# Performance work log

Measured on AMD Instinct MI355X. Metric: run time of the kernel, lower is better.

Reference implementation:

```python
import jax, jax.numpy as jnp
import numpy as np

NEURAL_DIM = 512
N_UNITS = 512
N_DAYS = 24
N_CLASSES = 41
N_LAYERS = 5
PATCH = 14
STRIDE = 4
MEMORY_SIZE = 256
IN0 = NEURAL_DIM * PATCH  # 7168, layer-0 input after patch concat


def _expm(M):
    """Matrix exponential via scaling-and-squaring + Taylor (float64 numpy)."""
    nrm = np.linalg.norm(M, 1)
    s = max(0, int(np.ceil(np.log2(nrm))) + 4) if nrm > 0 else 0
    Ms = M / (2.0 ** s)
    n = M.shape[0]
    E = np.eye(n)
    term = np.eye(n)
    for k in range(1, 25):
        term = term @ Ms / k
        E = E + term
    for _ in range(s):
        E = E @ E
    return E


def _lmu_AB(m_size):
    # NOTE: the torch cell calls _compute_A_B(memory_size, B.shape[0]), so the
    # effective theta used for discretization is memory_size itself.
    theta = float(m_size)
    q = np.arange(m_size, dtype=np.float64)
    R = ((2.0 * q + 1.0) / theta).reshape(-1, 1)
    i, j = np.meshgrid(q, q, indexing='ij')
    A = R * np.where(i < j, -1.0, (-1.0) ** (i - j + 1))
    Bc = R * ((-1.0) ** q).reshape(-1, 1)
    # zero-order hold discretization with dt=1: expm([[A,B],[0,0]])
    aug = np.zeros((m_size + 1, m_size + 1))
    aug[:m_size, :m_size] = A
    aug[:m_size, m_size:] = Bc
    E = _expm(aug)
    return (jnp.asarray(E[:m_size, :m_size], dtype=jnp.float32),
            jnp.asarray(E[:m_size, m_size:], dtype=jnp.float32))


A_MAT, B_MAT = _lmu_AB(MEMORY_SIZE)  # [M,M], [M,1]


def setup_inputs() -> dict:
    key = jax.random.key(0)
    ks = jax.random.split(key, 20)

    def rn(k, shape, scale):
        return jax.random.normal(k, shape, dtype=jnp.float32) * scale

    inp = {
        'x': jax.random.normal(ks[0], (32, 1024, NEURAL_DIM), dtype=jnp.float32),
        'day_idx': jax.random.randint(ks[1], (32,), 0, N_DAYS),
        # day-specific input layers (init: identity + zero bias; perturb slightly)
        'day_W': jnp.broadcast_to(jnp.eye(NEURAL_DIM, dtype=jnp.float32), (N_DAYS, NEURAL_DIM, NEURAL_DIM)) + rn(ks[2], (N_DAYS, NEURAL_DIM, NEURAL_DIM), 0.01),
        'day_b': rn(ks[3], (N_DAYS, 1, NEURAL_DIM), 0.01),
        # layer 0 (input 7168)
        'e_x0': rn(ks[4], (1, IN0), 1.0 / np.sqrt(IN0)),
        'W_x0': rn(ks[5], (N_UNITS, IN0), np.sqrt(2.0 / (IN0 + N_UNITS))),
        # layers 1..4 (input 512)
        'e_xr': rn(ks[6], (N_LAYERS - 1, 1, N_UNITS), 1.0 / np.sqrt(N_UNITS)),
        'W_xr': rn(ks[7], (N_LAYERS - 1, N_UNITS, N_UNITS), np.sqrt(1.0 / N_UNITS)),
        # shared-shape per-layer params (stacked over 5 layers)
        'e_h': rn(ks[8], (N_LAYERS, 1, N_UNITS), 1.0 / np.sqrt(N_UNITS)),
        'e_m': rn(ks[9], (N_LAYERS, 1, MEMORY_SIZE), 0.02),
        'W_h': rn(ks[10], (N_LAYERS, N_UNITS, N_UNITS), np.sqrt(1.0 / N_UNITS)),
        'W_m': rn(ks[11], (N_LAYERS, N_UNITS, MEMORY_SIZE), np.sqrt(2.0 / (MEMORY_SIZE + N_UNITS))),
        'h0': rn(ks[12], (N_LAYERS, 1, N_UNITS), 0.05),
        'm0': rn(ks[13], (N_LAYERS, 1, MEMORY_SIZE), 0.05),
        'out_W': rn(ks[14], (N_CLASSES, N_UNITS), np.sqrt(2.0 / (N_UNITS + N_CLASSES))),
        'out_b': jnp.zeros((N_CLASSES,), dtype=jnp.float32),
    }
    return inp


def _run_lmu_layer(seq, e_x, W_x, e_h, e_m, W_h, W_m, h_init, m_init):
    """seq: [B,T,in] -> [B,T,H] LMU recurrence."""
    # precompute input projections (the only big GEMMs) outside the scan
    xWx = jnp.einsum('bti,hi->bth', seq, W_x)   # [B,T,H]
    xex = jnp.einsum('bti,oi->bto', seq, e_x)   # [B,T,1]

    def step(carry, inp):
        h, m = carry
        xw, xe = inp
        u = xe + h @ e_h.T + m @ e_m.T          # [B,1]
        m = m @ A_MAT.T + u @ B_MAT.T           # [B,M]
        h = jnp.tanh(xw + h @ W_h.T + m @ W_m.T)
        return (h, m), h

    (_, _), hs = jax.lax.scan(step, (h_init, m_init),
                              (jnp.swapaxes(xWx, 0, 1), jnp.swapaxes(xex, 0, 1)))
    return jnp.swapaxes(hs, 0, 1)  # [B,T,H]


def reference(x, day_idx, day_W, day_b, e_x0, W_x0, e_xr, W_xr,
              e_h, e_m, W_h, W_m, h0, m0, out_W, out_b):
    B = x.shape[0]
    # day-specific linear + softsign
    h = jnp.einsum('btd,bdk->btk', x, day_W[day_idx]) + day_b[day_idx]
    h = h / (1.0 + jnp.abs(h))  # Softsign
    # patch concat: unfold time dim with window=PATCH, stride=STRIDE
    T = h.shape[1]
    Tp = (T - PATCH) // STRIDE + 1
    idx = jnp.arange(Tp)[:, None] * STRIDE + jnp.arange(PATCH)[None, :]
    h = h[:, idx, :].reshape(B, Tp, PATCH * NEURAL_DIM)  # [B,Tp,7168]

    bc = lambda v, d: jnp.broadcast_to(v, (B, d))
    seq = _run_lmu_layer(h, e_x0, W_x0, e_h[0], e_m[0], W_h[0], W_m[0],
                         bc(h0[0], N_UNITS), bc(m0[0], MEMORY_SIZE))
    for i in range(1, N_LAYERS):
        seq = _run_lmu_layer(seq, e_xr[i - 1], W_xr[i - 1], e_h[i], e_m[i],
                             W_h[i], W_m[i], bc(h0[i], N_UNITS), bc(m0[i], MEMORY_SIZE))
    logits = seq @ out_W.T + out_b  # [B,Tp,n_classes]
    return logits
```

## Files before the change

kernel.cpp:

```cpp
#include <hip/hip_runtime.h>
#include <hip/hip_fp16.h>

typedef _Float16 f16;
typedef _Float16 f16x8 __attribute__((ext_vector_type(8)));
typedef float f32x4 __attribute__((ext_vector_type(4)));

#define DI static __device__ __forceinline__

constexpr int N2 = 257 * 257;
#define LSTRIDE ((size_t)254 * 32 * 768)

DI f32x4 mfma16(f16x8 a, f16x8 b, f32x4 c) {
  return __builtin_amdgcn_mfma_f32_16x16x32_f16(a, b, c, 0, 0, 0);
}
DI f16x8 ldg8(const f16* p) { return *reinterpret_cast<const f16x8*>(p); }
DI f16x8 cvt8(const float* s) {
  f16x8 v;
#pragma unroll
  for (int j = 0; j < 8; ++j) v[j] = (f16)s[j];
  return v;
}
DI double invfact(int k) {
  double f = 1.0;
  for (int i = 2; i <= k; ++i) f *= (double)i;
  return 1.0 / f;
}

DI void st_d_sc1(double* p, double v) {
  asm volatile("global_store_dwordx2 %0, %1, off sc1" :: "v"(p), "v"(v) : "memory");
}
DI void st_f_sc1(float* p, float v) {
  asm volatile("global_store_dword %0, %1, off sc1" :: "v"(p), "v"(v) : "memory");
}
DI void st_h_sc1(f16* p, f16 v) {
  asm volatile("global_store_short %0, %1, off sc1" :: "v"(p), "v"(v) : "memory");
}
DI int ld_llc(const int* p) {
  return __hip_atomic_load(p, __ATOMIC_RELAXED, __HIP_MEMORY_SCOPE_AGENT);
}
DI void add_llc(int* p) {
  __hip_atomic_fetch_add(p, 1, __ATOMIC_RELAXED, __HIP_MEMORY_SCOPE_AGENT);
}
DI void drain_vm() { asm volatile("s_waitcnt vmcnt(0)" ::: "memory"); }
DI void membar() {
  __builtin_amdgcn_sched_barrier(0);
  asm volatile("" ::: "memory");
}
DI void spin_ge(const int* p, int target) {
  for (int it = 0; it < (1 << 14); ++it) {
    if (ld_llc(p) >= target) return;
    __builtin_amdgcn_s_sleep(1);
  }
}
DI void st4_sc1(f16* b, f16 v0, f16 v1, f16 v2, f16 v3) {
  const f16* b2 = b + 1536;
  asm volatile(
      "global_store_short %4, %0, off sc1\n\t"
      "global_store_short %4, %1, off offset:1536 sc1\n\t"
      "global_store_short %5, %2, off sc1\n\t"
      "global_store_short %5, %3, off offset:1536 sc1\n\t"
      "s_waitcnt vmcnt(0)"
      :: "v"(v0), "v"(v1), "v"(v2), "v"(v3), "v"(b), "v"(b2) : "memory");
}

DI void gridbar_nf(int* bar, int nwg) {
  drain_vm();
  __syncthreads();
  if (threadIdx.x == 0) {
    int g = ld_llc(bar + 1);
    int old = __hip_atomic_fetch_add(bar, 1, __ATOMIC_RELAXED, __HIP_MEMORY_SCOPE_AGENT);
    if (old == nwg - 1) {
      __hip_atomic_store(bar, 0, __ATOMIC_RELAXED, __HIP_MEMORY_SCOPE_AGENT);
      add_llc(bar + 1);
    } else {
      for (int it = 0; it < (1 << 14) && ld_llc(bar + 1) == g; ++it)
        __builtin_amdgcn_s_sleep(1);
    }
  }
  __syncthreads();
}

DI void mm257(double* __restrict__ D, const double* __restrict__ A, const double* __restrict__ Bm,
              int fj, const double* __restrict__ T1, const double* __restrict__ T2,
              const double* __restrict__ T3, int gtid, int nth) {
  double c0 = 0, c1 = 0, c2 = 0, c3 = 0;
  if (fj >= 0) {
    c0 = invfact(4 * fj); c1 = invfact(4 * fj + 1);
    c2 = invfact(4 * fj + 2); c3 = invfact(4 * fj + 3);
  }
  for (int e = gtid; e < N2; e += nth) {
    int i = e / 257, j = e - i * 257;
    const double* ar = A + (size_t)i * 257;
    const double* bc = Bm + j;
    double s0 = 0, s1 = 0, s2 = 0, s3 = 0;
    for (int k = 0; k < 256; k += 4) {
      s0 = fma(ar[k], bc[(size_t)k * 257], s0);
      s1 = fma(ar[k + 1], bc[(size_t)(k + 1) * 257], s1);
      s2 = fma(ar[k + 2], bc[(size_t)(k + 2) * 257], s2);
      s3 = fma(ar[k + 3], bc[(size_t)(k + 3) * 257], s3);
    }
    double s = ((s0 + s1) + (s2 + s3)) + ar[256] * bc[(size_t)256 * 257];
    if (fj >= 0) s += c0 * ((i == j) ? 1.0 : 0.0) + c1 * T1[e] + c2 * T2[e] + c3 * T3[e];
    st_d_sc1(D + e, s);
  }
}

__global__ __launch_bounds__(256) void k_setup(
    const float* __restrict__ dayW, const float* __restrict__ ex0, const float* __restrict__ Wx0,
    const float* __restrict__ exr, const float* __restrict__ Wxr,
    const float* __restrict__ eh, const float* __restrict__ em,
    const float* __restrict__ Wh, const float* __restrict__ Wm, const float* __restrict__ outW,
    double* __restrict__ X, float* __restrict__ w1f, float* __restrict__ AWt,
    float* __restrict__ btf, f16* __restrict__ gbuf, f16* __restrict__ wxcat,
    f16* __restrict__ outw, f16* __restrict__ dayWt, int* __restrict__ bar) {
  const int gtid = blockIdx.x * 256 + threadIdx.x;
  const int nth = 128 * 256;
  double* Ms = X;
  double* M2 = X + N2;
  double* M3 = X + 2 * N2;
  double* M4 = X + 3 * N2;
  double* H = X + 4 * N2;
  double* S = X + 11 * N2;

  for (int e = gtid; e < N2; e += nth) {
    int i = e / 257, j = e - i * 257;
    double v = 0.0;
    if (i < 256) {
      double R = (2.0 * i + 1.0) / 256.0;
      if (j < 256) v = R * ((i < j) ? -1.0 : (((i - j) & 1) ? 1.0 : -1.0));
      else v = R * ((i & 1) ? -1.0 : 1.0);
    }
    st_d_sc1(Ms + e, v / 64.0);
  }
  for (int e = gtid; e < 576 * 896; e += nth) {
    int n = e / 896, kc = (e - n * 896) * 8;
    f16x8 v;
    if (n < 512) v = cvt8(Wx0 + (size_t)n * 7168 + kc);
    else if (n == 512) v = cvt8(ex0 + kc);
    else {
#pragma unroll
      for (int j = 0; j < 8; ++j) v[j] = (f16)0.f;
    }
    *reinterpret_cast<f16x8*>(wxcat + (size_t)n * 7168 + kc) = v;
  }
  for (int e = gtid; e < 48 * 64; e += nth) {
    int n = e / 64, kc = (e - n * 64) * 8;
    f16x8 v;
    if (n < 41) v = cvt8(outW + (size_t)n * 512 + kc);
    else {
#pragma unroll
      for (int j = 0; j < 8; ++j) v[j] = (f16)0.f;
    }
    *reinterpret_cast<f16x8*>(outw + (size_t)n * 512 + kc) = v;
  }
  {
    __shared__ float tile[64][65];
    for (int tt = blockIdx.x; tt < 24 * 64; tt += 128) {
      int D = tt >> 6; int r = tt & 63; int kb = (r >> 3) * 64; int nb = (r & 7) * 64;
      __syncthreads();
      for (int q = 0; q < 16; ++q) {
        int idx = threadIdx.x + q * 256; int kk = idx >> 6; int nn = idx & 63;
        tile[kk][nn] = dayW[(size_t)D * 262144 + (size_t)(kb + kk) * 512 + nb + nn];
      }
      __syncthreads();
      for (int q = 0; q < 2; ++q) {
        int cidx = threadIdx.x + q * 256; int nn = cidx >> 3; int kc = (cidx & 7) * 8;
        f16x8 v;
#pragma unroll
        for (int jj = 0; jj < 8; ++jj) v[jj] = (f16)tile[kc + jj][nn];
        *reinterpret_cast<f16x8*>(dayWt + (size_t)D * 262144 + (size_t)(nb + nn) * 512 + kb + kc) = v;
      }
    }
    __syncthreads();
  }
  gridbar_nf(bar, 128);

  mm257(M2, Ms, Ms, -1, Ms, Ms, Ms, gtid, nth); gridbar_nf(bar, 128);
  mm257(M3, M2, Ms, -1, Ms, Ms, Ms, gtid, nth); gridbar_nf(bar, 128);
  mm257(M4, M2, M2, -1, Ms, Ms, Ms, gtid, nth);
  for (int e = gtid; e < N2; e += nth) {
    int i = e / 257, j = e - i * 257;
    st_d_sc1(H + e, (i == j) ? invfact(24) : 0.0);
  }
  gridbar_nf(bar, 128);
  for (int k = 0; k < 6; ++k) {
    mm257(H + (size_t)(k + 1) * N2, H + (size_t)k * N2, M4, 5 - k, Ms, M2, M3, gtid, nth);
    gridbar_nf(bar, 128);
  }
  {
    const double* Ssrc = H + (size_t)6 * N2;
    for (int k = 0; k < 6; ++k) {
      mm257(S + (size_t)k * N2, Ssrc, Ssrc, -1, Ms, Ms, Ms, gtid, nth);
      gridbar_nf(bar, 128);
      Ssrc = S + (size_t)k * N2;
    }
  }
  const double* E = S + (size_t)5 * N2;

  for (int e = gtid; e < 256; e += nth) st_f_sc1(btf + e, (float)E[(size_t)e * 257 + 256]);
  for (int e = gtid; e < 5 * 512; e += nth) {
    int l = e / 512, n = e - l * 512;
    const float* wm = Wm + ((size_t)l * 512 + n) * 256;
    float s = 0.f;
    for (int j = 0; j < 256; ++j) s += (float)E[(size_t)j * 257 + 256] * wm[j];
    st_f_sc1(w1f + e, s);
  }
  for (int e = gtid; e < 5 * 512 * 256; e += nth) {
    int l = e / (512 * 256); int r = e - l * 512 * 256; int n = r >> 8; int i = r & 255;
    const double* Ec = E + i;
    const float* wm = Wm + ((size_t)l * 512 + n) * 256;
    float s0 = 0, s1 = 0, s2 = 0, s3 = 0;
    for (int j = 0; j < 256; j += 4) {
      s0 += (float)Ec[(size_t)j * 257] * wm[j];
      s1 += (float)Ec[(size_t)(j + 1) * 257] * wm[j + 1];
      s2 += (float)Ec[(size_t)(j + 2) * 257] * wm[j + 2];
      s3 += (float)Ec[(size_t)(j + 3) * 257] * wm[j + 3];
    }
    st_f_sc1(AWt + e, (s0 + s1) + (s2 + s3));
  }
  gridbar_nf(bar, 128);

  for (int e = gtid; e < 5 * 768 * 160; e += nth) {
    int l = e / (768 * 160); int r = e - l * 768 * 160; int n = r / 160; int k = (r - n * 160) * 8;
    if (l == 0 && k >= 768) continue;
    f16x8 v;
    if (n < 512) {
      float w1n = w1f[l * 512 + n];
      if (k < 512) {
        const float* a = Wh + ((size_t)l * 512 + n) * 512 + k;
        const float* b = eh + (size_t)l * 512 + k;
#pragma unroll
        for (int jj = 0; jj < 8; ++jj) v[jj] = (f16)(a[jj] + b[jj] * w1n);
      } else if (k < 768) {
        int i = k - 512;
        const float* a = AWt + ((size_t)l * 512 + n) * 256 + i;
        const float* b = em + (size_t)l * 256 + i;
#pragma unroll
        for (int jj = 0; jj < 8; ++jj) v[jj] = (f16)(a[jj] + b[jj] * w1n);
      } else {
        int d = k - 768;
        const float* a = Wxr + ((size_t)(l - 1) * 512 + n) * 512 + d;
        const float* b = exr + (size_t)(l - 1) * 512 + d;
#pragma unroll
        for (int jj = 0; jj < 8; ++jj) v[jj] = (f16)(a[jj] + b[jj] * w1n);
      }
    } else {
      int jm = n - 512;
      float btn = btf[jm];
      if (k < 512) {
        const float* b = eh + (size_t)l * 512 + k;
#pragma unroll
        for (int jj = 0; jj < 8; ++jj) v[jj] = (f16)(b[jj] * btn);
      } else if (k < 768) {
        int i = k - 512;
        const double* a = E + (size_t)jm * 257 + i;
        const float* b = em + (size_t)l * 256 + i;
#pragma unroll
        for (int jj = 0; jj < 8; ++jj) v[jj] = (f16)((float)a[jj] + b[jj] * btn);
      } else {
        int d = k - 768;
        const float* b = exr + (size_t)(l - 1) * 512 + d;
#pragma unroll
        for (int jj = 0; jj < 8; ++jj) v[jj] = (f16)(b[jj] * btn);
      }
    }
    *reinterpret_cast<f16x8*>(gbuf + ((size_t)l * 768 + n) * 1280 + k) = v;
  }
}

__global__ __launch_bounds__(256) void k_day(const float* __restrict__ x,
    const int* __restrict__ dayIdx, const float* __restrict__ dayb,
    const f16* __restrict__ dayWt, f16* __restrict__ h1) {
  __shared__ f16 As[64][40];
  __shared__ f16 Bs[256][40];
  const int bid = blockIdx.x;
  const int b = bid >> 5; const int r = bid & 31;
  const int t0 = (r >> 1) * 64; const int n0 = (r & 1) * 256;
  const int D = dayIdx[b];
  const int tid = threadIdx.x, lane = tid & 63, w = tid >> 6, q4 = lane >> 4;
  const float* xb = x + ((size_t)b * 1024 + t0) * 512;
  const f16* Wt = dayWt + (size_t)D * 262144 + (size_t)n0 * 512;
  f32x4 acc[16];
#pragma unroll
  for (int i = 0; i < 16; ++i) acc[i] = (f32x4){0.f, 0.f, 0.f, 0.f};
  for (int kt = 0; kt < 16; ++kt) {
    const int k0 = kt * 32;
    __syncthreads();
    { int row = tid >> 2, c8 = (tid & 3) * 8;
      *reinterpret_cast<f16x8*>(&As[row][c8]) = cvt8(xb + (size_t)row * 512 + k0 + c8); }
    for (int q = 0; q < 4; ++q) {
      int idx = tid + q * 256; int row = idx >> 2; int c8 = (idx & 3) * 8;
      *reinterpret_cast<f16x8*>(&Bs[row][c8]) = ldg8(Wt + (size_t)row * 512 + k0 + c8);
    }
    __syncthreads();
    f16x8 a = *reinterpret_cast<const f16x8*>(&As[w * 16 + (lane & 15)][q4 * 8]);
#pragma unroll
    for (int nt2 = 0; nt2 < 16; ++nt2) {
      f16x8 bb = *reinterpret_cast<const f16x8*>(&Bs[nt2 * 16 + (lane & 15)][q4 * 8]);
      acc[nt2] = mfma16(a, bb, acc[nt2]);
    }
  }
#pragma unroll
  for (int nt2 = 0; nt2 < 16; ++nt2) {
    int n = n0 + nt2 * 16 + (lane & 15);
    float db = dayb[(size_t)D * 512 + n];
#pragma unroll
    for (int i = 0; i < 4; ++i) {
      int t = t0 + w * 16 + q4 * 4 + i;
      float v = acc[nt2][i] + db;
      v = v / (1.f + fabsf(v));
      h1[((size_t)b * 1024 + t) * 512 + n] = (f16)v;
    }
  }
}

__global__ __launch_bounds__(256) void k_xw0(const f16* __restrict__ h1,
    const f16* __restrict__ wxcat, float* __restrict__ xw0) {
  __shared__ f16 As[128][40];
  __shared__ f16 Bs[96][40];
  const int bid = blockIdx.x;
  const int mt = bid / 6; const int nb = bid - mt * 6;
  const int m0 = mt * 128; const int n0 = nb * 96;
  const int tid = threadIdx.x, lane = tid & 63, w = tid >> 6, q4 = lane >> 4;
  f32x4 acc[2][6];
#pragma unroll
  for (int a = 0; a < 2; ++a)
#pragma unroll
    for (int b = 0; b < 6; ++b) acc[a][b] = (f32x4){0.f, 0.f, 0.f, 0.f};
  for (int kt = 0; kt < 224; ++kt) {
    const int k0 = kt * 32; const int p = k0 >> 9; const int kd = k0 & 511;
    __syncthreads();
    for (int q = 0; q < 2; ++q) {
      int idx = tid + q * 256; int row = idx >> 2; int c8 = (idx & 3) * 8;
      int m = m0 + row; int b = m >> 8; int tp = m & 255; if (tp > 252) tp = 252;
      *reinterpret_cast<f16x8*>(&As[row][c8]) =
          ldg8(h1 + ((size_t)b * 1024 + (size_t)tp * 4 + p) * 512 + kd + c8);
    }
    for (int q = 0; q < 2; ++q) {
      int idx = tid + q * 256;
      if (idx < 384) {
        int row = idx >> 2; int c8 = (idx & 3) * 8;
        *reinterpret_cast<f16x8*>(&Bs[row][c8]) =
            ldg8(wxcat + (size_t)(n0 + row) * 7168 + k0 + c8);
      }
    }
    __syncthreads();
#pragma unroll
    for (int mb = 0; mb < 2; ++mb) {
      f16x8 a = *reinterpret_cast<const f16x8*>(&As[w * 32 + mb * 16 + (lane & 15)][q4 * 8]);
#pragma unroll
      for (int nt2 = 0; nt2 < 6; ++nt2) {
        f16x8 bb = *reinterpret_cast<const f16x8*>(&Bs[nt2 * 16 + (lane & 15)][q4 * 8]);
        acc[mb][nt2] = mfma16(a, bb, acc[mb][nt2]);
      }
    }
  }
#pragma unroll
  for (int mb = 0; mb < 2; ++mb)
#pragma unroll
    for (int nt2 = 0; nt2 < 6; ++nt2)
#pragma unroll
      for (int i = 0; i < 4; ++i) {
        int m = m0 + w * 32 + mb * 16 + q4 * 4 + i;
        int n = n0 + nt2 * 16 + (lane & 15);
        xw0[(size_t)m * 576 + n] = acc[mb][nt2][i];
      }
}

template <int KK>
DI void rec_run(int l, int c, int tid, const f16* __restrict__ gbuf, f16* __restrict__ sbuf,
                const float* __restrict__ xw0, const float* __restrict__ w1f,
                const float* __restrict__ btf, const float* __restrict__ h0,
                const float* __restrict__ m0, int* done, f16* bflds) {
  const int lane = tid & 63, w = tid >> 6;
  const int mb = w / 3, nt = w % 3;
  const int nbase = c * 48 + nt * 16;
  const int ncol = nbase + (lane & 15);
  const int q4 = lane >> 4;

  for (int r = tid; r < 32 * 48; r += 384) {
    int row = r / 48; int col = c * 48 + (r - row * 48);
    float v = (col < 512) ? h0[(size_t)l * 512 + col] : m0[(size_t)l * 256 + col - 512];
    st_h_sc1(sbuf + (size_t)l * LSTRIDE + (size_t)row * 768 + col, (f16)v);
  }

  const f16* gb = gbuf + ((size_t)l * 768 + ncol) * 1280 + (size_t)q4 * 8;
  constexpr int NREG = (KK > 32) ? 32 : KK;
  f16x8 bf[NREG];
#pragma unroll
  for (int kk = 0; kk < NREG; ++kk) bf[kk] = ldg8(gb + (size_t)kk * 32);
  if (KK == 40) {
#pragma unroll
    for (int kk = 32; kk < 40; ++kk) {
      f16x8 v = ldg8(gb + (size_t)kk * 32);
      *reinterpret_cast<f16x8*>(bflds + ((size_t)(w * 8 + (kk - 32)) * 64 + lane) * 8) = v;
    }
  }
  float w1n = 0.f, btn = 0.f;
  if (KK == 24) {
    if (ncol < 512) w1n = w1f[ncol];
    else btn = btf[ncol - 512];
  }
  drain_vm();
  __syncthreads();
  if (tid == 0) add_llc(done + l * 256);

  for (int t = 0; t < 253; ++t) {
    if (tid == 0) {
      spin_ge(done + l * 256 + t, 16);
      if (l > 0) spin_ge(done + (l - 1) * 256 + t + 1, 16);
    }
    __builtin_amdgcn_s_barrier();
    membar();

    const int arow = mb * 16 + (lane & 15);
    const f16* s0 = sbuf + (size_t)l * LSTRIDE + ((size_t)t * 32 + arow) * 768 + (size_t)q4 * 8;
    f32x4 acc = {0.f, 0.f, 0.f, 0.f};
#pragma unroll
    for (int kk = 0; kk < 24; ++kk) acc = mfma16(ldg8(s0 + (size_t)kk * 32), bf[kk < NREG ? kk : 0], acc);
    if (KK == 40) {
      const f16* s1 = sbuf + (size_t)(l - 1) * LSTRIDE + ((size_t)(t + 1) * 32 + arow) * 768 + (size_t)q4 * 8;
#pragma unroll
      for (int kk = 24; kk < 32; ++kk) acc = mfma16(ldg8(s1 + (size_t)(kk - 24) * 32), bf[kk < NREG ? kk : 0], acc);
#pragma unroll
      for (int kk = 32; kk < 40; ++kk) {
        f16x8 bb = *reinterpret_cast<const f16x8*>(bflds + ((size_t)(w * 8 + (kk - 32)) * 64 + lane) * 8);
        acc = mfma16(ldg8(s1 + (size_t)(kk - 24) * 32), bb, acc);
      }
    }

    f16 v4[4];
#pragma unroll
    for (int i = 0; i < 4; ++i) {
      const int brow = mb * 16 + q4 * 4 + i;
      float v = acc[i];
      if (KK == 24) {
        const float* xr = xw0 + ((size_t)brow * 256 + t) * 576;
        float xe = xr[512];
        v += (ncol < 512) ? (xr[ncol] + xe * w1n) : (xe * btn);
      }
      if (ncol < 512) v = tanhf(v);
      v4[i] = (f16)v;
    }
    f16* dst = sbuf + (size_t)l * LSTRIDE +
               ((size_t)(t + 1) * 32 + (size_t)(mb * 16 + q4 * 4)) * 768 + ncol;
    st4_sc1(dst, v4[0], v4[1], v4[2], v4[3]);

    __builtin_amdgcn_s_barrier();
    if (tid == 0) add_llc(done + l * 256 + t + 1);
  }
}

__global__ __launch_bounds__(384, 2) void k_rec(const f16* __restrict__ gbuf, f16* __restrict__ sbuf,
    const float* __restrict__ xw0, const float* __restrict__ w1f,
    const float* __restrict__ btf, const float* __restrict__ h0,
    const float* __restrict__ m0, int* __restrict__ done) {
  __shared__ f16 bflds[6 * 8 * 64 * 8];
  const int l = blockIdx.x >> 4;
  const int c = blockIdx.x & 15;
  if (l == 0)
    rec_run<24>(0, c, threadIdx.x, gbuf, sbuf, xw0, w1f, btf, h0, m0, done, bflds);
  else
    rec_run<40>(l, c, threadIdx.x, gbuf, sbuf, xw0, w1f, btf, h0, m0, done, bflds);
}

__global__ __launch_bounds__(256) void k_out(const f16* __restrict__ sbuf4,
    const f16* __restrict__ outw, const float* __restrict__ outb, float* __restrict__ out) {
  const int bid = blockIdx.x; const int b = bid >> 2; const int tp0 = (bid & 3) * 64;
  const int tid = threadIdx.x, lane = tid & 63, w = tid >> 6, q4 = lane >> 4;
  f32x4 acc[3];
#pragma unroll
  for (int i = 0; i < 3; ++i) acc[i] = (f32x4){0.f, 0.f, 0.f, 0.f};
  int tq = tp0 + w * 16 + (lane & 15) + 1;
  const int tau = tq > 253 ? 253 : tq;
  const f16* arow = sbuf4 + ((size_t)tau * 32 + b) * 768 + (size_t)q4 * 8;
#pragma unroll
  for (int kk = 0; kk < 16; ++kk) {
    f16x8 a = ldg8(arow + (size_t)kk * 32);
#pragma unroll
    for (int nt2 = 0; nt2 < 3; ++nt2) {
      f16x8 bb = ldg8(outw + (size_t)(nt2 * 16 + (lane & 15)) * 512 + kk * 32 + q4 * 8);
      acc[nt2] = mfma16(a, bb, acc[nt2]);
    }
  }
#pragma unroll
  for (int nt2 = 0; nt2 < 3; ++nt2) {
    int cc = nt2 * 16 + (lane & 15);
    if (cc < 41) {
      float ob = outb[cc];
#pragma unroll
      for (int i = 0; i < 4; ++i) {
        int tp = tp0 + w * 16 + q4 * 4 + i;
        if (tp < 253) out[((size_t)b * 253 + tp) * 41 + cc] = acc[nt2][i] + ob;
      }
    }
  }
}

extern "C" void kernel_launch(void* const* d_in, const int* in_sizes, int n_in,
                              void* d_out, int out_size, void* d_ws, size_t ws_size,
                              hipStream_t stream) {
  const float* x      = (const float*)d_in[0];
  const int*   dayIdx = (const int*)d_in[1];
  const float* day_W  = (const float*)d_in[2];
  const float* day_b  = (const float*)d_in[3];
  const float* e_x0   = (const float*)d_in[4];
  const float* W_x0   = (const float*)d_in[5];
  const float* e_xr   = (const float*)d_in[6];
  const float* W_xr   = (const float*)d_in[7];
  const float* e_h    = (const float*)d_in[8];
  const float* e_m    = (const float*)d_in[9];
  const float* W_h    = (const float*)d_in[10];
  const float* W_m    = (const float*)d_in[11];
  const float* h0     = (const float*)d_in[12];
  const float* m0     = (const float*)d_in[13];
  const float* out_W  = (const float*)d_in[14];
  const float* out_b  = (const float*)d_in[15];
  float* outp = (float*)d_out;

  char* w = (char*)d_ws;
  size_t o = 0;
  auto al = [&](size_t n) { void* p = w + o; o = (o + n + 255) & ~(size_t)255; return p; };

  int*   flags = (int*)  al(16384);
  f16*   gbuf  = (f16*)  al((size_t)5 * 768 * 1280 * 2);
  f16*   outw  = (f16*)  al((size_t)48 * 512 * 2);
  float* xw0   = (float*)al((size_t)8192 * 576 * 4);
  float* w1f   = (float*)al((size_t)5 * 512 * 4);
  float* btf   = (float*)al(256 * 4);

  const size_t XB    = ((size_t)17 * N2 * 8 + 255) & ~(size_t)255;
  const size_t AWTB  = ((size_t)5 * 512 * 256 * 4 + 255) & ~(size_t)255;
  const size_t DAYB  = ((size_t)24 * 512 * 512 * 2 + 255) & ~(size_t)255;
  const size_t WXB   = ((size_t)576 * 7168 * 2 + 255) & ~(size_t)255;
  const size_t H1B   = ((size_t)32 * 1024 * 512 * 2 + 255) & ~(size_t)255;
  const size_t SBUFB = (size_t)5 * LSTRIDE * 2;
  size_t ovb = XB + AWTB + DAYB + WXB + H1B;
  if (SBUFB > ovb) ovb = SBUFB;
  char* ov = (char*)al(ovb);
  double* X     = (double*)ov;
  float*  AWt   = (float*)(ov + XB);
  f16*    dayWt = (f16*)(ov + XB + AWTB);
  f16*    wxcat = (f16*)(ov + XB + AWTB + DAYB);
  f16*    h1    = (f16*)(ov + XB + AWTB + DAYB + WXB);
  f16*    sbuf  = (f16*)ov;

  if (o > ws_size) return;
  (void)in_sizes; (void)n_in; (void)out_size;

  hipMemsetAsync(flags, 0, 16384, stream);
  k_setup<<<128, 256, 0, stream>>>(day_W, e_x0, W_x0, e_xr, W_xr, e_h, e_m, W_h, W_m,
                                   out_W, X, w1f, AWt, btf, gbuf, wxcat, outw, dayWt,
                                   flags + 2048);
  k_day<<<1024, 256, 0, stream>>>(x, dayIdx, day_b, dayWt, h1);
  k_xw0<<<384, 256, 0, stream>>>(h1, wxcat, xw0);
  k_rec<<<80, 384, 0, stream>>>(gbuf, sbuf, xw0, w1f, btf, h0, m0, flags);
  k_out<<<128, 256, 0, stream>>>(sbuf + (size_t)4 * LSTRIDE, outw, out_b, outp);
}
```

Measured before the change: 4.252 ms.

## Replace atomic counter sync with per-block byte flags and coalesced tile stores

After: 4.101 ms. -3.5%, faster.

```diff
diff --git a/kernel.cpp b/kernel.cpp
--- a/kernel.cpp
+++ b/kernel.cpp
@@ -3,7 +3,9 @@
 
 typedef _Float16 f16;
 typedef _Float16 f16x8 __attribute__((ext_vector_type(8)));
+typedef _Float16 f16x4 __attribute__((ext_vector_type(4)));
 typedef float f32x4 __attribute__((ext_vector_type(4)));
+typedef int int4v __attribute__((ext_vector_type(4)));
 
 #define DI static __device__ __forceinline__
 
@@ -35,6 +37,13 @@
 DI void st_h_sc1(f16* p, f16 v) {
   asm volatile("global_store_short %0, %1, off sc1" :: "v"(p), "v"(v) : "memory");
 }
+DI void st_b_sc1(unsigned char* p, int v) {
+  asm volatile("global_store_byte %0, %1, off sc1" :: "v"(p), "v"(v) : "memory");
+}
+DI void st8_sc1(f16* p, f16x4 v) {
+  asm volatile("global_store_dwordx2 %0, %1, off sc1\n\ts_waitcnt vmcnt(0)"
+               :: "v"(p), "v"(v) : "memory");
+}
 DI int ld_llc(const int* p) {
   return __hip_atomic_load(p, __ATOMIC_RELAXED, __HIP_MEMORY_SCOPE_AGENT);
 }
@@ -46,21 +55,34 @@
   __builtin_amdgcn_sched_barrier(0);
   asm volatile("" ::: "memory");
 }
-DI void spin_ge(const int* p, int target) {
+DI bool all_one(int4v a) {
+  return a.x == 0x01010101 && a.y == 0x01010101 && a.z == 0x01010101 && a.w == 0x01010101;
+}
+DI void poll_one(const int* p) {
   for (int it = 0; it < (1 << 14); ++it) {
-    if (ld_llc(p) >= target) return;
+    int4v a;
+    asm volatile("global_load_dwordx4 %0, %1, off sc1\n\ts_waitcnt vmcnt(0)"
+                 : "=v"(a) : "v"(p) : "memory");
+    if (all_one(a)) return;
     __builtin_amdgcn_s_sleep(1);
   }
 }
-DI void st4_sc1(f16* b, f16 v0, f16 v1, f16 v2, f16 v3) {
-  const f16* b2 = b + 1536;
-  asm volatile(
-      "global_store_short %4, %0, off sc1\n\t"
-      "global_store_short %4, %1, off offset:1536 sc1\n\t"
-      "global_store_short %5, %2, off sc1\n\t"
-      "global_store_short %5, %3, off offset:1536 sc1\n\t"
-      "s_waitcnt vmcnt(0)"
-      :: "v"(v0), "v"(v1), "v"(v2), "v"(v3), "v"(b), "v"(b2) : "memory");
+DI void poll_two(const int* pa, const int* pb) {
+  for (int it = 0; it < (1 << 14); ++it) {
+    int4v a, b;
+    asm volatile(
+        "global_load_dwordx4 %0, %2, off sc1\n\t"
+        "global_load_dwordx4 %1, %3, off sc1\n\t"
+        "s_waitcnt vmcnt(0)"
+        : "=&v"(a), "=&v"(b) : "v"(pa), "v"(pb) : "memory");
+    if (all_one(a) && all_one(b)) return;
+    __builtin_amdgcn_s_sleep(1);
+  }
+}
+DI float tanh_fast(float x) {
+  x = fminf(9.f, fmaxf(-9.f, x));
+  float e = __expf(2.f * x);
+  return __fdividef(e - 1.f, e + 1.f);
 }
 
 DI void gridbar_nf(int* bar, int nwg) {
@@ -371,7 +393,7 @@
 DI void rec_run(int l, int c, int tid, const f16* __restrict__ gbuf, f16* __restrict__ sbuf,
                 const float* __restrict__ xw0, const float* __restrict__ w1f,
                 const float* __restrict__ btf, const float* __restrict__ h0,
-                const float* __restrict__ m0, int* done, f16* bflds) {
+                const float* __restrict__ m0, unsigned char* done, f16* bflds, f16* smtile) {
   const int lane = tid & 63, w = tid >> 6;
   const int mb = w / 3, nt = w % 3;
   const int nbase = c * 48 + nt * 16;
@@ -403,12 +425,23 @@
   }
   drain_vm();
   __syncthreads();
-  if (tid == 0) add_llc(done + l * 256);
+  if (tid == 0) st_b_sc1(done + (size_t)(l * 254) * 16 + c, 1);
 
   for (int t = 0; t < 253; ++t) {
+    float xadd[4];
+    if (KK == 24) {
+#pragma unroll
+      for (int i = 0; i < 4; ++i) {
+        const int brow = mb * 16 + q4 * 4 + i;
+        const float* xr = xw0 + ((size_t)brow * 256 + t) * 576;
+        float xe = xr[512];
+        xadd[i] = (ncol < 512) ? (xr[ncol] + xe * w1n) : (xe * btn);
+      }
+    }
     if (tid == 0) {
-      spin_ge(done + l * 256 + t, 16);
-      if (l > 0) spin_ge(done + (l - 1) * 256 + t + 1, 16);
+      const int* own = (const int*)(done + (size_t)(l * 254 + t) * 16);
+      if (l > 0) poll_two(own, (const int*)(done + (size_t)((l - 1) * 254 + t + 1) * 16));
+      else poll_one(own);
     }
     __builtin_amdgcn_s_barrier();
     membar();
@@ -429,39 +462,39 @@
       }
     }
 
-    f16 v4[4];
+    const int scol = nt * 16 + (lane & 15);
 #pragma unroll
     for (int i = 0; i < 4; ++i) {
-      const int brow = mb * 16 + q4 * 4 + i;
       float v = acc[i];
-      if (KK == 24) {
-        const float* xr = xw0 + ((size_t)brow * 256 + t) * 576;
-        float xe = xr[512];
-        v += (ncol < 512) ? (xr[ncol] + xe * w1n) : (xe * btn);
-      }
-      if (ncol < 512) v = tanhf(v);
-      v4[i] = (f16)v;
-    }
-    f16* dst = sbuf + (size_t)l * LSTRIDE +
-               ((size_t)(t + 1) * 32 + (size_t)(mb * 16 + q4 * 4)) * 768 + ncol;
-    st4_sc1(dst, v4[0], v4[1], v4[2], v4[3]);
-
+      if (KK == 24) v += xadd[i];
+      if (ncol < 512) v = tanh_fast(v);
+      smtile[(mb * 16 + q4 * 4 + i) * 48 + scol] = (f16)v;
+    }
+    __syncthreads();
+    {
+      int row = tid / 12; int c4 = (tid - row * 12) * 4;
+      f16x4 v4 = *reinterpret_cast<const f16x4*>(smtile + row * 48 + c4);
+      f16* dst = sbuf + (size_t)l * LSTRIDE + ((size_t)(t + 1) * 32 + row) * 768 + c * 48 + c4;
+      st8_sc1(dst, v4);
+    }
     __builtin_amdgcn_s_barrier();
-    if (tid == 0) add_llc(done + l * 256 + t + 1);
+    if (tid == 0) st_b_sc1(done + (size_t)(l * 254 + t + 1) * 16 + c, 1);
   }
 }
 
 __global__ __launch_bounds__(384, 2) void k_rec(const f16* __restrict__ gbuf, f16* __restrict__ sbuf,
     const float* __restrict__ xw0, const float* __restrict__ w1f,
     const float* __restrict__ btf, const float* __restrict__ h0,
-    const float* __restrict__ m0, int* __restrict__ done) {
+    const float* __restrict__ m0, unsigned char* __restrict__ done) {
   __shared__ f16 bflds[6 * 8 * 64 * 8];
-  const int l = blockIdx.x >> 4;
-  const int c = blockIdx.x & 15;
+  __shared__ f16 smtile[32 * 48];
+  const int l = blockIdx.x & 7;
+  if (l >= 5) return;
+  const int c = blockIdx.x >> 3;
   if (l == 0)
-    rec_run<24>(0, c, threadIdx.x, gbuf, sbuf, xw0, w1f, btf, h0, m0, done, bflds);
+    rec_run<24>(0, c, threadIdx.x, gbuf, sbuf, xw0, w1f, btf, h0, m0, done, bflds, smtile);
   else
-    rec_run<40>(l, c, threadIdx.x, gbuf, sbuf, xw0, w1f, btf, h0, m0, done, bflds);
+    rec_run<40>(l, c, threadIdx.x, gbuf, sbuf, xw0, w1f, btf, h0, m0, done, bflds, smtile);
 }
 
 __global__ __launch_bounds__(256) void k_out(const f16* __restrict__ sbuf4,
@@ -522,7 +555,7 @@
   size_t o = 0;
   auto al = [&](size_t n) { void* p = w + o; o = (o + n + 255) & ~(size_t)255; return p; };
 
-  int*   flags = (int*)  al(16384);
+  int*   flags = (int*)  al(32768);
   f16*   gbuf  = (f16*)  al((size_t)5 * 768 * 1280 * 2);
   f16*   outw  = (f16*)  al((size_t)48 * 512 * 2);
   float* xw0   = (float*)al((size_t)8192 * 576 * 4);
@@ -548,12 +581,12 @@
   if (o > ws_size) return;
   (void)in_sizes; (void)n_in; (void)out_size;
 
-  hipMemsetAsync(flags, 0, 16384, stream);
+  hipMemsetAsync(flags, 0, 32768, stream);
   k_setup<<<128, 256, 0, stream>>>(day_W, e_x0, W_x0, e_xr, W_xr, e_h, e_m, W_h, W_m,
                                    out_W, X, w1f, AWt, btf, gbuf, wxcat, outw, dayWt,
-                                   flags + 2048);
+                                   flags + 6144);
   k_day<<<1024, 256, 0, stream>>>(x, dayIdx, day_b, dayWt, h1);
   k_xw0<<<384, 256, 0, stream>>>(h1, wxcat, xw0);
-  k_rec<<<80, 384, 0, stream>>>(gbuf, sbuf, xw0, w1f, btf, h0, m0, flags);
+  k_rec<<<128, 384, 0, stream>>>(gbuf, sbuf, xw0, w1f, btf, h0, m0, (unsigned char*)flags);
   k_out<<<128, 256, 0, stream>>>(sbuf + (size_t)4 * LSTRIDE, outw, out_b, outp);
 }
```
